# Kernel tuning notes

Measured on AMD Instinct MI355X. Metric: run time of the kernel, lower is better.

## Reference

```python
import jax, jax.numpy as jnp
import numpy as np

NUM_HEADS = 4


def _conv1x1(W, b, x):
    # nn.Conv1d(d_model, d_model, kernel_size=1): pointwise channel mix
    return jnp.einsum('oi,bin->bon', W, x) + b[None, :, None]


def _rot3d_rel_position(desc0, pos, lrf):
    # desc0: [b, d, h, n_pts], pos: [b, n, m, 3], lrf: [b, n, 3, 3] (n == n_pts == m)
    b, d, h, npts = desc0.shape
    m = pos.shape[2]
    # rotate-half: pairs (x0, x1) -> (-x1, x0)
    dh = desc0.reshape(b, d // 2, 2, h, npts)
    desc = jnp.concatenate([-dh[:, :, 1:2], dh[:, :, 0:1]], axis=2).reshape(b, d, h, npts)
    # rotate relative positions into each point's local reference frame
    # torch: einsum('bnxy,bnmy->bnmx', lrf.transpose(2,3), pos) == einsum('bnyx,bnmy->bnmx', lrf, pos)
    posl = jnp.einsum('bnyx,bnmy->bnmx', lrf, pos)
    px, py, pz = posl[..., 0], posl[..., 1], posl[..., 2]
    alpha = jnp.arctan(py / px)
    alpha = jnp.where(px < 0, alpha + np.pi, alpha)
    phi = jnp.arctan(pz / jnp.sqrt(px * px + py * py))
    alpha = jnp.where(jnp.isnan(alpha), 0.0, alpha)
    phi = jnp.where(jnp.isnan(phi), 0.0, phi)
    # F.interpolate(nearest, [m,4]) on [b,n,m,2] duplicates the last axis: [a,a,p,p]
    rot = jnp.stack([alpha, alpha, phi, phi], axis=-1)      # [b,n,m,4]
    rot = jnp.tile(rot, (1, 1, 1, d // 4))                  # [b,n,m,d] (head-independent)
    # 5D rotated value tensor (faithful to original math; head axis broadcast)
    return (jnp.einsum('bdhn,bnmd->bdhnm', desc0, jnp.cos(rot))
            + jnp.einsum('bdhn,bnmd->bdhnm', desc, jnp.sin(rot)))


def setup_inputs() -> dict:
    key = jax.random.key(0)
    ks = jax.random.split(key, 13)
    b, d_model, n, m = 4, 256, 256, 256
    s = 1.0 / np.sqrt(d_model)
    inp = {
        'x': jax.random.normal(ks[0], (b, d_model, n), dtype=jnp.float32),
        'source': jax.random.normal(ks[1], (b, d_model, m), dtype=jnp.float32),
        'x_pos': jax.random.normal(ks[2], (b, n, 3), dtype=jnp.float32),
        'src_pos': jax.random.normal(ks[3], (b, m, 3), dtype=jnp.float32),
        'lrf': jax.random.normal(ks[4], (b, n, 3, 3), dtype=jnp.float32),
        'Wq': jax.random.normal(ks[5], (d_model, d_model), dtype=jnp.float32) * s,
        'bq': jax.random.normal(ks[6], (d_model,), dtype=jnp.float32) * 0.02,
        'Wk': jax.random.normal(ks[7], (d_model, d_model), dtype=jnp.float32) * s,
        'bk': jax.random.normal(ks[8], (d_model,), dtype=jnp.float32) * 0.02,
        'Wv': jax.random.normal(ks[9], (d_model, d_model), dtype=jnp.float32) * s,
        'bv': jax.random.normal(ks[10], (d_model,), dtype=jnp.float32) * 0.02,
        'Wm': jax.random.normal(ks[11], (d_model, d_model), dtype=jnp.float32) * s,
        'bm': jax.random.normal(ks[12], (d_model,), dtype=jnp.float32) * 0.02,
        'k': 32,
    }
    return inp


def reference(x, source, x_pos, src_pos, lrf, Wq, bq, Wk, bk, Wv, bv, Wm, bm, k):
    b, d_model, n = x.shape
    m = source.shape[2]
    h = NUM_HEADS
    dim = d_model // h
    q = _conv1x1(Wq, bq, x).reshape(b, dim, h, n)
    key_ = _conv1x1(Wk, bk, source).reshape(b, dim, h, m)
    val = _conv1x1(Wv, bv, source).reshape(b, dim, h, m)
    # 'self' branch: 3D rotary relative-position encoding of values
    rel = x_pos[:, :, None, :] - src_pos[:, None, :, :]  # [b,n,m,3]
    value5 = _rot3d_rel_position(val, rel, lrf)          # [b,dim,h,n,m]
    # dynamic (top-k sparsified) attention
    scores = jnp.einsum('bdhn,bdhm->bhnm', q, key_) / np.float32(dim) ** 0.5
    vals, idx = jax.lax.top_k(scores, k)                 # over key axis m
    probs = jax.nn.softmax(vals, axis=-1)
    bi = jnp.arange(b)[:, None, None, None]
    hi = jnp.arange(h)[None, :, None, None]
    ni = jnp.arange(n)[None, None, :, None]
    sparse = jnp.zeros_like(scores).at[bi, hi, ni, idx].set(probs)
    # note the deliberate m<->n swap on value5 as in the original einsum
    out = jnp.einsum('bhnm,bdhmn->bdhn', sparse, value5)
    return _conv1x1(Wm, bm, out.reshape(b, d_model, n))
```

## Files before the change

kernel.cpp:

```cpp
#include <hip/hip_runtime.h>
#include <math.h>

#define DM 256
#define NP 256
#define NH 4
#define DH 64

typedef unsigned long long u64;
typedef unsigned int u32;

__global__ __launch_bounds__(256) void qkv_proj_kernel(
    const float* __restrict__ x, const float* __restrict__ src,
    const float* __restrict__ Wq, const float* __restrict__ bq,
    const float* __restrict__ Wk, const float* __restrict__ bk,
    const float* __restrict__ Wv, const float* __restrict__ bv,
    float* __restrict__ Qt, float* __restrict__ Kt, float* __restrict__ Vt)
{
  const int tile = blockIdx.x;
  const int mat  = blockIdx.y;
  const int b    = blockIdx.z;
  const int tc = (tile >> 2) * 64;
  const int tp = (tile & 3) * 64;
  const float* W    = (mat == 0) ? Wq : (mat == 1) ? Wk : Wv;
  const float* bias = (mat == 0) ? bq : (mat == 1) ? bk : bv;
  const float* X    = ((mat == 0) ? x : src) + (size_t)b * DM * NP;
  float* T          = ((mat == 0) ? Qt : (mat == 1) ? Kt : Vt) + (size_t)b * NH * NP * DH;

  __shared__ float Ws[2][32][64];
  __shared__ float Xs[2][32][64];
  const int tid = threadIdx.x;
  const int ty = tid >> 4, tx = tid & 15;
  const int c0 = tid >> 3;
  const int k4 = tid & 7;
  const int pX = tid & 15;
  const int kX = tid >> 4;

  float4 wA, wB, xA, xB;
  #define LOADQKV(K0)                                                          \
    wA = *(const float4*)&W[(size_t)(tc + c0)      * DM + (K0) + k4 * 4];      \
    wB = *(const float4*)&W[(size_t)(tc + c0 + 32) * DM + (K0) + k4 * 4];      \
    xA = *(const float4*)&X[(size_t)((K0) + kX)      * NP + tp + pX * 4];      \
    xB = *(const float4*)&X[(size_t)((K0) + kX + 16) * NP + tp + pX * 4];

  #define STOREQKV(BUF)                                                        \
    Ws[BUF][k4*4+0][c0] = wA.x; Ws[BUF][k4*4+1][c0] = wA.y;                    \
    Ws[BUF][k4*4+2][c0] = wA.z; Ws[BUF][k4*4+3][c0] = wA.w;                    \
    Ws[BUF][k4*4+0][c0+32] = wB.x; Ws[BUF][k4*4+1][c0+32] = wB.y;              \
    Ws[BUF][k4*4+2][c0+32] = wB.z; Ws[BUF][k4*4+3][c0+32] = wB.w;              \
    *(float4*)&Xs[BUF][kX][pX*4]      = xA;                                    \
    *(float4*)&Xs[BUF][kX+16][pX*4]   = xB;

  LOADQKV(0);
  STOREQKV(0);
  __syncthreads();

  float acc[4][4];
  #pragma unroll
  for (int i = 0; i < 4; ++i)
    #pragma unroll
    for (int j = 0; j < 4; ++j) acc[i][j] = 0.f;

  for (int ch = 0; ch < 8; ++ch) {
    const int cur = ch & 1;
    if (ch < 7) { LOADQKV((ch + 1) * 32); }
    #pragma unroll
    for (int kk = 0; kk < 32; ++kk) {
      float4 a = *(const float4*)&Ws[cur][kk][ty * 4];
      float4 xv = *(const float4*)&Xs[cur][kk][tx * 4];
      float av[4] = {a.x, a.y, a.z, a.w};
      float xvv[4] = {xv.x, xv.y, xv.z, xv.w};
      #pragma unroll
      for (int i = 0; i < 4; ++i)
        #pragma unroll
        for (int j = 0; j < 4; ++j) acc[i][j] += av[i] * xvv[j];
    }
    if (ch < 7) {
      STOREQKV(cur ^ 1);
      __syncthreads();
    }
  }

  #pragma unroll
  for (int i = 0; i < 4; ++i) {
    const int c = tc + ty * 4 + i;
    const float bb = bias[c];
    #pragma unroll
    for (int j = 0; j < 4; ++j) {
      const int p = tp + tx * 4 + j;
      T[((size_t)(c & 3) * NP + p) * DH + (c >> 2)] = acc[i][j] + bb;
    }
  }
  #undef LOADQKV
  #undef STOREQKV
}

__global__ __launch_bounds__(256) void score_gemm_kernel(
    const float* __restrict__ Qt, const float* __restrict__ Kt,
    float* __restrict__ scores)
{
  const int tile = blockIdx.x;
  const int bh   = blockIdx.y;
  const int tn = (tile >> 2) * 64;
  const int tm = (tile & 3) * 64;
  const float* Qb = Qt + (size_t)bh * NP * DH;
  const float* Kb = Kt + (size_t)bh * NP * DH;

  __shared__ float Qs[64][68];
  __shared__ float Ks[64][68];
  const int tid = threadIdx.x;

  #pragma unroll
  for (int p = 0; p < 4; ++p) {
    const int u = tid + p * 256;
    const int r = u >> 4;
    const int g = u & 15;
    const float4 qv = *(const float4*)&Qb[(size_t)(tn + r) * DH + g * 4];
    const float4 kv = *(const float4*)&Kb[(size_t)(tm + r) * DH + g * 4];
    Qs[g*4+0][r] = qv.x; Qs[g*4+1][r] = qv.y;
    Qs[g*4+2][r] = qv.z; Qs[g*4+3][r] = qv.w;
    Ks[g*4+0][r] = kv.x; Ks[g*4+1][r] = kv.y;
    Ks[g*4+2][r] = kv.z; Ks[g*4+3][r] = kv.w;
  }
  __syncthreads();

  const int ty = tid >> 4, tx = tid & 15;
  float acc[4][4];
  #pragma unroll
  for (int i = 0; i < 4; ++i)
    #pragma unroll
    for (int j = 0; j < 4; ++j) acc[i][j] = 0.f;

  #pragma unroll 4
  for (int d = 0; d < DH; ++d) {
    const float4 a = *(const float4*)&Qs[d][ty * 4];
    const float4 bv = *(const float4*)&Ks[d][tx * 4];
    const float av[4] = {a.x, a.y, a.z, a.w};
    const float bvv[4] = {bv.x, bv.y, bv.z, bv.w};
    #pragma unroll
    for (int i = 0; i < 4; ++i)
      #pragma unroll
      for (int j = 0; j < 4; ++j) acc[i][j] += av[i] * bvv[j];
  }

  float* srow = scores + ((size_t)bh * NP + tn) * NP + tm;
  #pragma unroll
  for (int i = 0; i < 4; ++i) {
    float4 o4;
    o4.x = acc[i][0] * 0.125f; o4.y = acc[i][1] * 0.125f;
    o4.z = acc[i][2] * 0.125f; o4.w = acc[i][3] * 0.125f;
    *(float4*)&srow[(size_t)(ty * 4 + i) * NP + tx * 4] = o4;
  }
}

__global__ __launch_bounds__(256) void attn_topk_kernel(
    const float* __restrict__ scores, const float* __restrict__ Vt,
    const float* __restrict__ x_pos, const float* __restrict__ src_pos,
    const float* __restrict__ lrf,
    const int* __restrict__ kptr,
    float* __restrict__ O)
{
  const int tid  = threadIdx.x;
  const int wid  = tid >> 6;
  const int lane = tid & 63;
  const int bidx = blockIdx.x;
  const int rb   = (bidx & 7) * 128 + (bidx >> 3);
  const int row  = rb * 4 + wid;
  const int n    = row & (NP - 1);
  const int bh   = row >> 8;
  const int b    = bh >> 2;
  const int h    = bh & 3;

  int kk = *kptr;
  if (kk > 64) kk = 64;
  if (kk < 1) kk = 1;

  __shared__ float  eslot[4][64];
  __shared__ int    msel[4][64];
  __shared__ float4 ang[4][64];
  __shared__ float  otile[4][64];

  const float4 s4 = *(const float4*)&scores[(size_t)row * NP + lane * 4];
  float s[4] = { s4.x, s4.y, s4.z, s4.w };
  u32 u[4], lowv[4];
  #pragma unroll
  for (int r = 0; r < 4; ++r) {
    u32 bb = __float_as_uint(s[r]);
    u[r] = (bb & 0x80000000u) ? ~bb : (bb | 0x80000000u);
    lowv[r] = (u32)(255 - (lane * 4 + r));
  }

  u32 T = 0u;
  #pragma unroll
  for (int bit = 31; bit >= 0; --bit) {
    const u32 cand = T | (1u << bit);
    int c = 0;
    #pragma unroll
    for (int r = 0; r < 4; ++r) c += __popcll(__ballot(u[r] >= cand));
    if (c >= kk) T = cand;
  }
  int c_gt = 0;
  #pragma unroll
  for (int r = 0; r < 4; ++r) c_gt += __popcll(__ballot(u[r] > T));

  u32 Lo = 0u;
  #pragma unroll
  for (int bit = 7; bit >= 0; --bit) {
    const u32 cand = Lo | (1u << bit);
    int c = c_gt;
    #pragma unroll
    for (int r = 0; r < 4; ++r)
      c += __popcll(__ballot((u[r] == T) && (lowv[r] >= cand)));
    if (c >= kk) Lo = cand;
  }

  const float sT = __uint_as_float((T & 0x80000000u) ? (T & 0x7fffffffu) : ~T);
  bool sel[4]; float e[4]; u64 selm[4];
  #pragma unroll
  for (int r = 0; r < 4; ++r) {
    sel[r] = (u[r] > T) || ((u[r] == T) && (lowv[r] >= Lo));
    e[r] = sel[r] ? expf(s[r] - sT) : 0.f;
    selm[r] = __ballot(sel[r]);
  }
  float z = e[0] + e[1] + e[2] + e[3];
  #pragma unroll
  for (int off = 32; off; off >>= 1) z += __shfl_xor(z, off);

  const u64 lt = (1ull << lane) - 1ull;
  int base = 0;
  #pragma unroll
  for (int r = 0; r < 4; ++r) {
    if (sel[r]) {
      const int slot = base + __popcll(selm[r] & lt);
      eslot[wid][slot] = e[r];
      msel[wid][slot]  = lane * 4 + r;
    }
    base += __popcll(selm[r]);
  }

  if (lane < kk) {
    const float ej = eslot[wid][lane];
    const int   mj = msel[wid][lane];
    const float p = ej / z;
    const float* xp = x_pos   + ((size_t)b * NP + mj) * 3;
    const float* sp = src_pos + ((size_t)b * NP + n) * 3;
    const float* L  = lrf     + ((size_t)b * NP + mj) * 9;
    const float r0 = xp[0] - sp[0], r1 = xp[1] - sp[1], r2v = xp[2] - sp[2];
    const float px = L[0]*r0 + L[3]*r1 + L[6]*r2v;
    const float py = L[1]*r0 + L[4]*r1 + L[7]*r2v;
    const float pz = L[2]*r0 + L[5]*r1 + L[8]*r2v;
    const float r2 = px*px + py*py;
    const float inv2 = (r2 > 0.f) ? rsqrtf(r2) : 0.f;
    const float ca = (r2 > 0.f) ? px * inv2 : 1.f;
    const float sa = py * inv2;
    const float r2d = r2 * inv2;
    const float r3 = r2 + pz * pz;
    const float inv3 = (r3 > 0.f) ? rsqrtf(r3) : 0.f;
    const float cph = (r3 > 0.f) ? r2d * inv3 : 1.f;
    const float sph = pz * inv3;
    ang[wid][lane] = make_float4(p * ca, p * sa, p * cph, p * sph);
  }

  const float* vbase = Vt + (size_t)bh * NP * DH;
  const bool useA = ((lane & 3) < 2);
  const bool odd  = (lane & 1);
  const int  ev   = lane & ~1;
  float acc = 0.f;

  int j = 0;
  for (; j + 4 <= kk; j += 4) {
    const int ma = msel[wid][j],   mb = msel[wid][j+1];
    const int mc = msel[wid][j+2], md = msel[wid][j+3];
    const float4 Aa = ang[wid][j],   Ab = ang[wid][j+1];
    const float4 Ac = ang[wid][j+2], Ad = ang[wid][j+3];
    const float2 va = *(const float2*)(vbase + (size_t)ma * DH + ev);
    const float2 vb = *(const float2*)(vbase + (size_t)mb * DH + ev);
    const float2 vc = *(const float2*)(vbase + (size_t)mc * DH + ev);
    const float2 vd = *(const float2*)(vbase + (size_t)md * DH + ev);
    float vm, dsc, pc, ps;
    vm = odd ? va.y : va.x;  dsc = odd ? va.x : -va.y;
    pc = useA ? Aa.x : Aa.z; ps  = useA ? Aa.y : Aa.w;
    acc += vm * pc + dsc * ps;
    vm = odd ? vb.y : vb.x;  dsc = odd ? vb.x : -vb.y;
    pc = useA ? Ab.x : Ab.z; ps  = useA ? Ab.y : Ab.w;
    acc += vm * pc + dsc * ps;
    vm = odd ? vc.y : vc.x;  dsc = odd ? vc.x : -vc.y;
    pc = useA ? Ac.x : Ac.z; ps  = useA ? Ac.y : Ac.w;
    acc += vm * pc + dsc * ps;
    vm = odd ? vd.y : vd.x;  dsc = odd ? vd.x : -vd.y;
    pc = useA ? Ad.x : Ad.z; ps  = useA ? Ad.y : Ad.w;
    acc += vm * pc + dsc * ps;
  }
  for (; j < kk; ++j) {
    const int m = msel[wid][j];
    const float4 A = ang[wid][j];
    const float2 v2 = *(const float2*)(vbase + (size_t)m * DH + ev);
    const float vm  = odd ? v2.y :  v2.x;
    const float dsc = odd ? v2.x : -v2.y;
    acc += vm * (useA ? A.x : A.z) + dsc * (useA ? A.y : A.w);
  }

  otile[wid][lane] = acc;
  __syncthreads();
  if (wid == 0) {
    float4 o4;
    o4.x = otile[0][lane]; o4.y = otile[1][lane];
    o4.z = otile[2][lane]; o4.w = otile[3][lane];
    const int c = (lane << 2) | h;
    const int n0 = (rb * 4) & (NP - 1);
    *(float4*)&O[((size_t)b * DM + c) * NP + n0] = o4;
  }
}

__global__ __launch_bounds__(256) void final_proj_kernel(
    const float* __restrict__ O, const float* __restrict__ Wm,
    const float* __restrict__ bm, float* __restrict__ out)
{
  const int tile = blockIdx.x;
  const int b    = blockIdx.y;
  const int tc = (tile >> 2) * 64;
  const int tp = (tile & 3) * 64;
  const float* X = O + (size_t)b * DM * NP;
  float* Y       = out + (size_t)b * DM * NP;

  __shared__ float Ws[2][32][64];
  __shared__ float Xs[2][32][64];
  const int tid = threadIdx.x;
  const int ty = tid >> 4, tx = tid & 15;
  const int c0 = tid >> 3;
  const int k4 = tid & 7;
  const int pX = tid & 15;
  const int kX = tid >> 4;

  float4 wA, wB, xA, xB;
  #define LOADF(K0)                                                            \
    wA = *(const float4*)&Wm[(size_t)(tc + c0)      * DM + (K0) + k4 * 4];     \
    wB = *(const float4*)&Wm[(size_t)(tc + c0 + 32) * DM + (K0) + k4 * 4];     \
    xA = *(const float4*)&X[(size_t)((K0) + kX)      * NP + tp + pX * 4];      \
    xB = *(const float4*)&X[(size_t)((K0) + kX + 16) * NP + tp + pX * 4];

  #define STOREF(BUF)                                                          \
    Ws[BUF][k4*4+0][c0] = wA.x; Ws[BUF][k4*4+1][c0] = wA.y;                    \
    Ws[BUF][k4*4+2][c0] = wA.z; Ws[BUF][k4*4+3][c0] = wA.w;                    \
    Ws[BUF][k4*4+0][c0+32] = wB.x; Ws[BUF][k4*4+1][c0+32] = wB.y;              \
    Ws[BUF][k4*4+2][c0+32] = wB.z; Ws[BUF][k4*4+3][c0+32] = wB.w;              \
    *(float4*)&Xs[BUF][kX][pX*4]      = xA;                                    \
    *(float4*)&Xs[BUF][kX+16][pX*4]   = xB;

  LOADF(0);
  STOREF(0);
  __syncthreads();

  float acc[4][4];
  #pragma unroll
  for (int i = 0; i < 4; ++i)
    #pragma unroll
    for (int j = 0; j < 4; ++j) acc[i][j] = 0.f;

  for (int ch = 0; ch < 8; ++ch) {
    const int cur = ch & 1;
    if (ch < 7) { LOADF((ch + 1) * 32); }
    #pragma unroll
    for (int kk = 0; kk < 32; ++kk) {
      float4 a = *(const float4*)&Ws[cur][kk][ty * 4];
      float4 xv = *(const float4*)&Xs[cur][kk][tx * 4];
      float av[4] = {a.x, a.y, a.z, a.w};
      float xvv[4] = {xv.x, xv.y, xv.z, xv.w};
      #pragma unroll
      for (int i = 0; i < 4; ++i)
        #pragma unroll
        for (int j = 0; j < 4; ++j) acc[i][j] += av[i] * xvv[j];
    }
    if (ch < 7) {
      STOREF(cur ^ 1);
      __syncthreads();
    }
  }

  #pragma unroll
  for (int i = 0; i < 4; ++i) {
    const int c = tc + ty * 4 + i;
    const float bb = bm[c];
    float4 o4;
    o4.x = acc[i][0] + bb; o4.y = acc[i][1] + bb;
    o4.z = acc[i][2] + bb; o4.w = acc[i][3] + bb;
    *(float4*)&Y[(size_t)c * NP + tp + tx * 4] = o4;
  }
  #undef LOADF
  #undef STOREF
}

extern "C" void kernel_launch(void* const* d_in, const int* in_sizes, int n_in,
                              void* d_out, int out_size, void* d_ws, size_t ws_size,
                              hipStream_t stream)
{
  const float* x       = (const float*)d_in[0];
  const float* source  = (const float*)d_in[1];
  const float* x_pos   = (const float*)d_in[2];
  const float* src_pos = (const float*)d_in[3];
  const float* lrf     = (const float*)d_in[4];
  const float* Wq = (const float*)d_in[5];
  const float* bq = (const float*)d_in[6];
  const float* Wk = (const float*)d_in[7];
  const float* bk = (const float*)d_in[8];
  const float* Wv = (const float*)d_in[9];
  const float* bv = (const float*)d_in[10];
  const float* Wm = (const float*)d_in[11];
  const float* bm = (const float*)d_in[12];
  const int* kptr = (const int*)d_in[13];
  float* out = (float*)d_out;

  float* ws = (float*)d_ws;
  float* Qt = ws;
  float* Kt = Qt + 262144;
  float* Vt = Kt + 262144;
  float* O  = Vt + 262144;
  float* scores = O + 262144;

  qkv_proj_kernel<<<dim3(16, 3, 4), 256, 0, stream>>>(
      x, source, Wq, bq, Wk, bk, Wv, bv, Qt, Kt, Vt);
  score_gemm_kernel<<<dim3(16, 16), 256, 0, stream>>>(
      Qt, Kt, scores);
  attn_topk_kernel<<<dim3(1024), 256, 0, stream>>>(
      scores, Vt, x_pos, src_pos, lrf, kptr, O);
  final_proj_kernel<<<dim3(16, 4), 256, 0, stream>>>(
      O, Wm, bm, out);
}
```

Measured before the change: 52.46 us.

## Fuse four kernels into one persistent kernel with grid-wide barriers

Replaces the four separate launches (QKV projection, score GEMM, top-k attention, output projection) with one 256-block persistent kernel that separates phases with atomic-counter grid barriers, and a union of shared-memory layouts per phase. The aim is to remove inter-kernel launch gaps and tail effects. It also retiles the final projection to 32x32 tiles so it spans all 256 blocks, skips the tie-break bit search when there are no ties, and reuses the Qt buffer for O. The cost is a memset launch plus spin-wait barriers, which assume all 256 blocks are co-resident and can deadlock if they are not.

```diff
diff --git a/kernel.cpp b/kernel.cpp
--- a/kernel.cpp
+++ b/kernel.cpp
@@ -5,388 +5,387 @@
 #define NP 256
 #define NH 4
 #define DH 64
+#define NBLK 256
 
 typedef unsigned long long u64;
 typedef unsigned int u32;
 
-__global__ __launch_bounds__(256) void qkv_proj_kernel(
+union SMem {
+  struct { float Ws[2][32][64]; float Xs[2][32][64]; } p1;
+  struct { float Qs[64][68]; float Ks[64][68]; } p2;
+  struct { float eslot[4][64]; int msel[4][64];
+           float4 ang[4][64]; float otile[4][64]; } p3;
+  struct { float Wc[2][32][32]; float Xc[2][32][32]; } p4;
+};
+
+__device__ __forceinline__ void grid_barrier(int* bar, int idx) {
+  __syncthreads();
+  if (threadIdx.x == 0) {
+    __threadfence();
+    atomicAdd(&bar[idx], 1);
+    while (__hip_atomic_load(&bar[idx], __ATOMIC_ACQUIRE,
+                             __HIP_MEMORY_SCOPE_AGENT) < NBLK) { }
+  }
+  __syncthreads();
+  __threadfence();
+}
+
+__global__ __launch_bounds__(256, 1) void mega_kernel(
     const float* __restrict__ x, const float* __restrict__ src,
     const float* __restrict__ Wq, const float* __restrict__ bq,
     const float* __restrict__ Wk, const float* __restrict__ bk,
     const float* __restrict__ Wv, const float* __restrict__ bv,
-    float* __restrict__ Qt, float* __restrict__ Kt, float* __restrict__ Vt)
+    const float* __restrict__ Wm, const float* __restrict__ bm,
+    const float* __restrict__ x_pos, const float* __restrict__ src_pos,
+    const float* __restrict__ lrf, const int* __restrict__ kptr,
+    float* __restrict__ Qt, float* __restrict__ Kt, float* __restrict__ Vt,
+    float* __restrict__ scores, float* __restrict__ O,
+    int* __restrict__ bar,
+    float* __restrict__ out)
 {
-  const int tile = blockIdx.x;
-  const int mat  = blockIdx.y;
-  const int b    = blockIdx.z;
-  const int tc = (tile >> 2) * 64;
-  const int tp = (tile & 3) * 64;
-  const float* W    = (mat == 0) ? Wq : (mat == 1) ? Wk : Wv;
-  const float* bias = (mat == 0) ? bq : (mat == 1) ? bk : bv;
-  const float* X    = ((mat == 0) ? x : src) + (size_t)b * DM * NP;
-  float* T          = ((mat == 0) ? Qt : (mat == 1) ? Kt : Vt) + (size_t)b * NH * NP * DH;
-
-  __shared__ float Ws[2][32][64];
-  __shared__ float Xs[2][32][64];
+  __shared__ SMem S;
   const int tid = threadIdx.x;
-  const int ty = tid >> 4, tx = tid & 15;
-  const int c0 = tid >> 3;
-  const int k4 = tid & 7;
-  const int pX = tid & 15;
-  const int kX = tid >> 4;
-
-  float4 wA, wB, xA, xB;
-  #define LOADQKV(K0)                                                          \
-    wA = *(const float4*)&W[(size_t)(tc + c0)      * DM + (K0) + k4 * 4];      \
-    wB = *(const float4*)&W[(size_t)(tc + c0 + 32) * DM + (K0) + k4 * 4];      \
-    xA = *(const float4*)&X[(size_t)((K0) + kX)      * NP + tp + pX * 4];      \
-    xB = *(const float4*)&X[(size_t)((K0) + kX + 16) * NP + tp + pX * 4];
-
-  #define STOREQKV(BUF)                                                        \
-    Ws[BUF][k4*4+0][c0] = wA.x; Ws[BUF][k4*4+1][c0] = wA.y;                    \
-    Ws[BUF][k4*4+2][c0] = wA.z; Ws[BUF][k4*4+3][c0] = wA.w;                    \
-    Ws[BUF][k4*4+0][c0+32] = wB.x; Ws[BUF][k4*4+1][c0+32] = wB.y;              \
-    Ws[BUF][k4*4+2][c0+32] = wB.z; Ws[BUF][k4*4+3][c0+32] = wB.w;              \
-    *(float4*)&Xs[BUF][kX][pX*4]      = xA;                                    \
-    *(float4*)&Xs[BUF][kX+16][pX*4]   = xB;
-
-  LOADQKV(0);
-  STOREQKV(0);
-  __syncthreads();
-
-  float acc[4][4];
-  #pragma unroll
-  for (int i = 0; i < 4; ++i)
+  const int bid = blockIdx.x;
+
+  if (bid < 192) {
+    const int tile = bid & 15;
+    const int r    = bid >> 4;
+    const int mat  = r % 3;
+    const int b    = r / 3;
+    const int tc = (tile >> 2) * 64;
+    const int tp = (tile & 3) * 64;
+    const float* W    = (mat == 0) ? Wq : (mat == 1) ? Wk : Wv;
+    const float* bias = (mat == 0) ? bq : (mat == 1) ? bk : bv;
+    const float* X    = ((mat == 0) ? x : src) + (size_t)b * DM * NP;
+    float* T          = ((mat == 0) ? Qt : (mat == 1) ? Kt : Vt)
+                        + (size_t)b * NH * NP * DH;
+
+    const int ty = tid >> 4, tx = tid & 15;
+    const int c0 = tid >> 3;
+    const int k4 = tid & 7;
+    const int pX = tid & 15;
+    const int kX = tid >> 4;
+
+    float4 wA, wB, xA, xB;
+    #define LOADQKV(K0)                                                        \
+      wA = *(const float4*)&W[(size_t)(tc + c0)      * DM + (K0) + k4 * 4];    \
+      wB = *(const float4*)&W[(size_t)(tc + c0 + 32) * DM + (K0) + k4 * 4];    \
+      xA = *(const float4*)&X[(size_t)((K0) + kX)      * NP + tp + pX * 4];    \
+      xB = *(const float4*)&X[(size_t)((K0) + kX + 16) * NP + tp + pX * 4];
+    #define STOREQKV(BUF)                                                      \
+      S.p1.Ws[BUF][k4*4+0][c0] = wA.x; S.p1.Ws[BUF][k4*4+1][c0] = wA.y;        \
+      S.p1.Ws[BUF][k4*4+2][c0] = wA.z; S.p1.Ws[BUF][k4*4+3][c0] = wA.w;        \
+      S.p1.Ws[BUF][k4*4+0][c0+32] = wB.x; S.p1.Ws[BUF][k4*4+1][c0+32] = wB.y;  \
+      S.p1.Ws[BUF][k4*4+2][c0+32] = wB.z; S.p1.Ws[BUF][k4*4+3][c0+32] = wB.w;  \
+      *(float4*)&S.p1.Xs[BUF][kX][pX*4]    = xA;                               \
+      *(float4*)&S.p1.Xs[BUF][kX+16][pX*4] = xB;
+
+    LOADQKV(0);
+    STOREQKV(0);
+    __syncthreads();
+
+    float acc[4][4];
     #pragma unroll
-    for (int j = 0; j < 4; ++j) acc[i][j] = 0.f;
-
-  for (int ch = 0; ch < 8; ++ch) {
-    const int cur = ch & 1;
-    if (ch < 7) { LOADQKV((ch + 1) * 32); }
+    for (int i = 0; i < 4; ++i)
+      #pragma unroll
+      for (int j = 0; j < 4; ++j) acc[i][j] = 0.f;
+
+    for (int ch = 0; ch < 8; ++ch) {
+      const int cur = ch & 1;
+      if (ch < 7) { LOADQKV((ch + 1) * 32); }
+      #pragma unroll
+      for (int kx = 0; kx < 32; ++kx) {
+        float4 a  = *(const float4*)&S.p1.Ws[cur][kx][ty * 4];
+        float4 xv = *(const float4*)&S.p1.Xs[cur][kx][tx * 4];
+        float av[4]  = {a.x, a.y, a.z, a.w};
+        float xvv[4] = {xv.x, xv.y, xv.z, xv.w};
+        #pragma unroll
+        for (int i = 0; i < 4; ++i)
+          #pragma unroll
+          for (int j = 0; j < 4; ++j) acc[i][j] += av[i] * xvv[j];
+      }
+      if (ch < 7) {
+        STOREQKV(cur ^ 1);
+        __syncthreads();
+      }
+    }
+
     #pragma unroll
-    for (int kk = 0; kk < 32; ++kk) {
-      float4 a = *(const float4*)&Ws[cur][kk][ty * 4];
-      float4 xv = *(const float4*)&Xs[cur][kk][tx * 4];
-      float av[4] = {a.x, a.y, a.z, a.w};
-      float xvv[4] = {xv.x, xv.y, xv.z, xv.w};
+    for (int i = 0; i < 4; ++i) {
+      const int c = tc + ty * 4 + i;
+      const float bb = bias[c];
+      #pragma unroll
+      for (int j = 0; j < 4; ++j) {
+        const int p = tp + tx * 4 + j;
+        T[((size_t)(c & 3) * NP + p) * DH + (c >> 2)] = acc[i][j] + bb;
+      }
+    }
+    #undef LOADQKV
+    #undef STOREQKV
+  }
+
+  grid_barrier(bar, 0);
+
+  {
+    const int tile = bid & 15;
+    const int bh   = bid >> 4;
+    const int tn = (tile >> 2) * 64;
+    const int tm = (tile & 3) * 64;
+    const float* Qb = Qt + (size_t)bh * NP * DH;
+    const float* Kb = Kt + (size_t)bh * NP * DH;
+
+    #pragma unroll
+    for (int p = 0; p < 4; ++p) {
+      const int u = tid + p * 256;
+      const int r = u >> 4;
+      const int g = u & 15;
+      const float4 qv = *(const float4*)&Qb[(size_t)(tn + r) * DH + g * 4];
+      const float4 kv = *(const float4*)&Kb[(size_t)(tm + r) * DH + g * 4];
+      S.p2.Qs[g*4+0][r] = qv.x; S.p2.Qs[g*4+1][r] = qv.y;
+      S.p2.Qs[g*4+2][r] = qv.z; S.p2.Qs[g*4+3][r] = qv.w;
+      S.p2.Ks[g*4+0][r] = kv.x; S.p2.Ks[g*4+1][r] = kv.y;
+      S.p2.Ks[g*4+2][r] = kv.z; S.p2.Ks[g*4+3][r] = kv.w;
+    }
+    __syncthreads();
+
+    const int ty = tid >> 4, tx = tid & 15;
+    float acc[4][4];
+    #pragma unroll
+    for (int i = 0; i < 4; ++i)
+      #pragma unroll
+      for (int j = 0; j < 4; ++j) acc[i][j] = 0.f;
+
+    #pragma unroll 4
+    for (int d = 0; d < DH; ++d) {
+      const float4 a  = *(const float4*)&S.p2.Qs[d][ty * 4];
+      const float4 bv = *(const float4*)&S.p2.Ks[d][tx * 4];
+      const float av[4]  = {a.x, a.y, a.z, a.w};
+      const float bvv[4] = {bv.x, bv.y, bv.z, bv.w};
       #pragma unroll
       for (int i = 0; i < 4; ++i)
         #pragma unroll
-        for (int j = 0; j < 4; ++j) acc[i][j] += av[i] * xvv[j];
-    }
-    if (ch < 7) {
-      STOREQKV(cur ^ 1);
+        for (int j = 0; j < 4; ++j) acc[i][j] += av[i] * bvv[j];
+    }
+
+    float* srow = scores + ((size_t)bh * NP + tn) * NP + tm;
+    #pragma unroll
+    for (int i = 0; i < 4; ++i) {
+      float4 o4;
+      o4.x = acc[i][0] * 0.125f; o4.y = acc[i][1] * 0.125f;
+      o4.z = acc[i][2] * 0.125f; o4.w = acc[i][3] * 0.125f;
+      *(float4*)&srow[(size_t)(ty * 4 + i) * NP + tx * 4] = o4;
+    }
+  }
+
+  grid_barrier(bar, 1);
+
+  {
+    const int wid  = tid >> 6;
+    const int lane = tid & 63;
+    int kk = *kptr;
+    if (kk > 64) kk = 64;
+    if (kk < 1) kk = 1;
+
+    for (int sweep = 0; sweep < 4; ++sweep) {
+      const int rb  = sweep * 256 + bid;
+      const int row = rb * 4 + wid;
+      const int n   = row & (NP - 1);
+      const int bh  = row >> 8;
+      const int b   = bh >> 2;
+      const int h   = bh & 3;
+
+      const float4 s4 = *(const float4*)&scores[(size_t)row * NP + lane * 4];
+      float s[4] = { s4.x, s4.y, s4.z, s4.w };
+      u32 u[4], lowv[4];
+      #pragma unroll
+      for (int r = 0; r < 4; ++r) {
+        u32 bb = __float_as_uint(s[r]);
+        u[r] = (bb & 0x80000000u) ? ~bb : (bb | 0x80000000u);
+        lowv[r] = (u32)(255 - (lane * 4 + r));
+      }
+
+      u32 T = 0u;
+      #pragma unroll
+      for (int bit = 31; bit >= 0; --bit) {
+        const u32 cand = T | (1u << bit);
+        int c = 0;
+        #pragma unroll
+        for (int r = 0; r < 4; ++r) c += __popcll(__ballot(u[r] >= cand));
+        if (c >= kk) T = cand;
+      }
+      int c_gt = 0, c_ge = 0;
+      #pragma unroll
+      for (int r = 0; r < 4; ++r) {
+        c_gt += __popcll(__ballot(u[r] > T));
+        c_ge += __popcll(__ballot(u[r] >= T));
+      }
+
+      u32 Lo = 0u;
+      if (c_ge > kk) {
+        #pragma unroll
+        for (int bit = 7; bit >= 0; --bit) {
+          const u32 cand = Lo | (1u << bit);
+          int c = c_gt;
+          #pragma unroll
+          for (int r = 0; r < 4; ++r)
+            c += __popcll(__ballot((u[r] == T) && (lowv[r] >= cand)));
+          if (c >= kk) Lo = cand;
+        }
+      }
+
+      const float sT = __uint_as_float((T & 0x80000000u) ? (T & 0x7fffffffu) : ~T);
+      bool sel[4]; float e[4]; u64 selm[4];
+      #pragma unroll
+      for (int r = 0; r < 4; ++r) {
+        sel[r] = (u[r] > T) || ((u[r] == T) && (lowv[r] >= Lo));
+        e[r] = sel[r] ? expf(s[r] - sT) : 0.f;
+        selm[r] = __ballot(sel[r]);
+      }
+      float z = e[0] + e[1] + e[2] + e[3];
+      #pragma unroll
+      for (int off = 32; off; off >>= 1) z += __shfl_xor(z, off);
+
+      const u64 lt = (1ull << lane) - 1ull;
+      int base = 0;
+      #pragma unroll
+      for (int r = 0; r < 4; ++r) {
+        if (sel[r]) {
+          const int slot = base + __popcll(selm[r] & lt);
+          S.p3.eslot[wid][slot] = e[r];
+          S.p3.msel[wid][slot]  = lane * 4 + r;
+        }
+        base += __popcll(selm[r]);
+      }
+
+      if (lane < kk) {
+        const float ej = S.p3.eslot[wid][lane];
+        const int   mj = S.p3.msel[wid][lane];
+        const float p = ej / z;
+        const float* xp = x_pos   + ((size_t)b * NP + mj) * 3;
+        const float* sp = src_pos + ((size_t)b * NP + n) * 3;
+        const float* L  = lrf     + ((size_t)b * NP + mj) * 9;
+        const float r0 = xp[0] - sp[0], r1 = xp[1] - sp[1], r2v = xp[2] - sp[2];
+        const float px = L[0]*r0 + L[3]*r1 + L[6]*r2v;
+        const float py = L[1]*r0 + L[4]*r1 + L[7]*r2v;
+        const float pz = L[2]*r0 + L[5]*r1 + L[8]*r2v;
+        const float r2 = px*px + py*py;
+        const float inv2 = (r2 > 0.f) ? rsqrtf(r2) : 0.f;
+        const float ca = (r2 > 0.f) ? px * inv2 : 1.f;
+        const float sa = py * inv2;
+        const float r2d = r2 * inv2;
+        const float r3 = r2 + pz * pz;
+        const float inv3 = (r3 > 0.f) ? rsqrtf(r3) : 0.f;
+        const float cph = (r3 > 0.f) ? r2d * inv3 : 1.f;
+        const float sph = pz * inv3;
+        S.p3.ang[wid][lane] = make_float4(p * ca, p * sa, p * cph, p * sph);
+      }
+
+      const float* vbase = Vt + (size_t)bh * NP * DH;
+      const bool useA = ((lane & 3) < 2);
+      const bool odd  = (lane & 1);
+      const int  ev   = lane & ~1;
+      float acc = 0.f;
+
+      int j = 0;
+      for (; j + 4 <= kk; j += 4) {
+        const int ma = S.p3.msel[wid][j],   mb2 = S.p3.msel[wid][j+1];
+        const int mc = S.p3.msel[wid][j+2], md = S.p3.msel[wid][j+3];
+        const float4 Aa = S.p3.ang[wid][j],   Ab = S.p3.ang[wid][j+1];
+        const float4 Ac = S.p3.ang[wid][j+2], Ad = S.p3.ang[wid][j+3];
+        const float2 va = *(const float2*)(vbase + (size_t)ma  * DH + ev);
+        const float2 vb = *(const float2*)(vbase + (size_t)mb2 * DH + ev);
+        const float2 vc = *(const float2*)(vbase + (size_t)mc  * DH + ev);
+        const float2 vd = *(const float2*)(vbase + (size_t)md  * DH + ev);
+        float vm, dsc, pc, ps;
+        vm = odd ? va.y : va.x;  dsc = odd ? va.x : -va.y;
+        pc = useA ? Aa.x : Aa.z; ps  = useA ? Aa.y : Aa.w;
+        acc += vm * pc + dsc * ps;
+        vm = odd ? vb.y : vb.x;  dsc = odd ? vb.x : -vb.y;
+        pc = useA ? Ab.x : Ab.z; ps  = useA ? Ab.y : Ab.w;
+        acc += vm * pc + dsc * ps;
+        vm = odd ? vc.y : vc.x;  dsc = odd ? vc.x : -vc.y;
+        pc = useA ? Ac.x : Ac.z; ps  = useA ? Ac.y : Ac.w;
+        acc += vm * pc + dsc * ps;
+        vm = odd ? vd.y : vd.x;  dsc = odd ? vd.x : -vd.y;
+        pc = useA ? Ad.x : Ad.z; ps  = useA ? Ad.y : Ad.w;
+        acc += vm * pc + dsc * ps;
+      }
+      for (; j < kk; ++j) {
+        const int m = S.p3.msel[wid][j];
+        const float4 A = S.p3.ang[wid][j];
+        const float2 v2 = *(const float2*)(vbase + (size_t)m * DH + ev);
+        const float vm  = odd ? v2.y :  v2.x;
+        const float dsc = odd ? v2.x : -v2.y;
+        acc += vm * (useA ? A.x : A.z) + dsc * (useA ? A.y : A.w);
+      }
+
+      S.p3.otile[wid][lane] = acc;
       __syncthreads();
+      if (wid == 0) {
+        float4 o4;
+        o4.x = S.p3.otile[0][lane]; o4.y = S.p3.otile[1][lane];
+        o4.z = S.p3.otile[2][lane]; o4.w = S.p3.otile[3][lane];
+        const int c = (lane << 2) | h;
+        const int n0 = (rb * 4) & (NP - 1);
+        *(float4*)&O[((size_t)b * DM + c) * NP + n0] = o4;
+      }
+      __syncthreads();
     }
   }
 
-  #pragma unroll
-  for (int i = 0; i < 4; ++i) {
-    const int c = tc + ty * 4 + i;
-    const float bb = bias[c];
-    #pragma unroll
-    for (int j = 0; j < 4; ++j) {
-      const int p = tp + tx * 4 + j;
-      T[((size_t)(c & 3) * NP + p) * DH + (c >> 2)] = acc[i][j] + bb;
-    }
+  grid_barrier(bar, 2);
+
+  {
+    const int tp = (bid & 7) * 32;
+    const int tc = ((bid >> 3) & 7) * 32;
+    const int b  = bid >> 6;
+    const float* X = O + (size_t)b * DM * NP;
+    float* Y       = out + (size_t)b * DM * NP;
+
+    const int c0w = tid >> 3, kg = tid & 7;
+    const int krx = tid >> 3, pg = tid & 7;
+    const int ty = tid >> 4, tx = tid & 15;
+
+    float4 wv4, xv4;
+    #define LOADP4(K0)                                                         \
+      wv4 = *(const float4*)&Wm[(size_t)(tc + c0w) * DM + (K0) + kg * 4];      \
+      xv4 = *(const float4*)&X[(size_t)((K0) + krx) * NP + tp + pg * 4];
+    #define STOREP4(BUF)                                                       \
+      S.p4.Wc[BUF][kg*4+0][c0w] = wv4.x; S.p4.Wc[BUF][kg*4+1][c0w] = wv4.y;    \
+      S.p4.Wc[BUF][kg*4+2][c0w] = wv4.z; S.p4.Wc[BUF][kg*4+3][c0w] = wv4.w;    \
+      *(float4*)&S.p4.Xc[BUF][krx][pg*4] = xv4;
+
+    LOADP4(0);
+    STOREP4(0);
+    __syncthreads();
+
+    float a00 = 0.f, a01 = 0.f, a10 = 0.f, a11 = 0.f;
+    for (int ch = 0; ch < 8; ++ch) {
+      const int cur = ch & 1;
+      if (ch < 7) { LOADP4((ch + 1) * 32); }
+      #pragma unroll
+      for (int kx = 0; kx < 32; ++kx) {
+        const float2 wv = *(const float2*)&S.p4.Wc[cur][kx][ty * 2];
+        const float2 xv = *(const float2*)&S.p4.Xc[cur][kx][tx * 2];
+        a00 += wv.x * xv.x; a01 += wv.x * xv.y;
+        a10 += wv.y * xv.x; a11 += wv.y * xv.y;
+      }
+      if (ch < 7) {
+        STOREP4(cur ^ 1);
+        __syncthreads();
+      }
+    }
+
+    const int c = tc + ty * 2;
+    const int p = tp + tx * 2;
+    const float b0 = bm[c], b1 = bm[c + 1];
+    float2 o0 = make_float2(a00 + b0, a01 + b0);
+    float2 o1 = make_float2(a10 + b1, a11 + b1);
+    *(float2*)&Y[(size_t)c       * NP + p] = o0;
+    *(float2*)&Y[(size_t)(c + 1) * NP + p] = o1;
+    #undef LOADP4
+    #undef STOREP4
   }
-  #undef LOADQKV
-  #undef STOREQKV
-}
-
-__global__ __launch_bounds__(256) void score_gemm_kernel(
-    const float* __restrict__ Qt, const float* __restrict__ Kt,
-    float* __restrict__ scores)
-{
-  const int tile = blockIdx.x;
-  const int bh   = blockIdx.y;
-  const int tn = (tile >> 2) * 64;
-  const int tm = (tile & 3) * 64;
-  const float* Qb = Qt + (size_t)bh * NP * DH;
-  const float* Kb = Kt + (size_t)bh * NP * DH;
-
-  __shared__ float Qs[64][68];
-  __shared__ float Ks[64][68];
-  const int tid = threadIdx.x;
-
-  #pragma unroll
-  for (int p = 0; p < 4; ++p) {
-    const int u = tid + p * 256;
-    const int r = u >> 4;
-    const int g = u & 15;
-    const float4 qv = *(const float4*)&Qb[(size_t)(tn + r) * DH + g * 4];
-    const float4 kv = *(const float4*)&Kb[(size_t)(tm + r) * DH + g * 4];
-    Qs[g*4+0][r] = qv.x; Qs[g*4+1][r] = qv.y;
-    Qs[g*4+2][r] = qv.z; Qs[g*4+3][r] = qv.w;
-    Ks[g*4+0][r] = kv.x; Ks[g*4+1][r] = kv.y;
-    Ks[g*4+2][r] = kv.z; Ks[g*4+3][r] = kv.w;
-  }
-  __syncthreads();
-
-  const int ty = tid >> 4, tx = tid & 15;
-  float acc[4][4];
-  #pragma unroll
-  for (int i = 0; i < 4; ++i)
-    #pragma unroll
-    for (int j = 0; j < 4; ++j) acc[i][j] = 0.f;
-
-  #pragma unroll 4
-  for (int d = 0; d < DH; ++d) {
-    const float4 a = *(const float4*)&Qs[d][ty * 4];
-    const float4 bv = *(const float4*)&Ks[d][tx * 4];
-    const float av[4] = {a.x, a.y, a.z, a.w};
-    const float bvv[4] = {bv.x, bv.y, bv.z, bv.w};
-    #pragma unroll
-    for (int i = 0; i < 4; ++i)
-      #pragma unroll
-      for (int j = 0; j < 4; ++j) acc[i][j] += av[i] * bvv[j];
-  }
-
-  float* srow = scores + ((size_t)bh * NP + tn) * NP + tm;
-  #pragma unroll
-  for (int i = 0; i < 4; ++i) {
-    float4 o4;
-    o4.x = acc[i][0] * 0.125f; o4.y = acc[i][1] * 0.125f;
-    o4.z = acc[i][2] * 0.125f; o4.w = acc[i][3] * 0.125f;
-    *(float4*)&srow[(size_t)(ty * 4 + i) * NP + tx * 4] = o4;
-  }
-}
-
-__global__ __launch_bounds__(256) void attn_topk_kernel(
-    const float* __restrict__ scores, const float* __restrict__ Vt,
-    const float* __restrict__ x_pos, const float* __restrict__ src_pos,
-    const float* __restrict__ lrf,
-    const int* __restrict__ kptr,
-    float* __restrict__ O)
-{
-  const int tid  = threadIdx.x;
-  const int wid  = tid >> 6;
-  const int lane = tid & 63;
-  const int bidx = blockIdx.x;
-  const int rb   = (bidx & 7) * 128 + (bidx >> 3);
-  const int row  = rb * 4 + wid;
-  const int n    = row & (NP - 1);
-  const int bh   = row >> 8;
-  const int b    = bh >> 2;
-  const int h    = bh & 3;
-
-  int kk = *kptr;
-  if (kk > 64) kk = 64;
-  if (kk < 1) kk = 1;
-
-  __shared__ float  eslot[4][64];
-  __shared__ int    msel[4][64];
-  __shared__ float4 ang[4][64];
-  __shared__ float  otile[4][64];
-
-  const float4 s4 = *(const float4*)&scores[(size_t)row * NP + lane * 4];
-  float s[4] = { s4.x, s4.y, s4.z, s4.w };
-  u32 u[4], lowv[4];
-  #pragma unroll
-  for (int r = 0; r < 4; ++r) {
-    u32 bb = __float_as_uint(s[r]);
-    u[r] = (bb & 0x80000000u) ? ~bb : (bb | 0x80000000u);
-    lowv[r] = (u32)(255 - (lane * 4 + r));
-  }
-
-  u32 T = 0u;
-  #pragma unroll
-  for (int bit = 31; bit >= 0; --bit) {
-    const u32 cand = T | (1u << bit);
-    int c = 0;
-    #pragma unroll
-    for (int r = 0; r < 4; ++r) c += __popcll(__ballot(u[r] >= cand));
-    if (c >= kk) T = cand;
-  }
-  int c_gt = 0;
-  #pragma unroll
-  for (int r = 0; r < 4; ++r) c_gt += __popcll(__ballot(u[r] > T));
-
-  u32 Lo = 0u;
-  #pragma unroll
-  for (int bit = 7; bit >= 0; --bit) {
-    const u32 cand = Lo | (1u << bit);
-    int c = c_gt;
-    #pragma unroll
-    for (int r = 0; r < 4; ++r)
-      c += __popcll(__ballot((u[r] == T) && (lowv[r] >= cand)));
-    if (c >= kk) Lo = cand;
-  }
-
-  const float sT = __uint_as_float((T & 0x80000000u) ? (T & 0x7fffffffu) : ~T);
-  bool sel[4]; float e[4]; u64 selm[4];
-  #pragma unroll
-  for (int r = 0; r < 4; ++r) {
-    sel[r] = (u[r] > T) || ((u[r] == T) && (lowv[r] >= Lo));
-    e[r] = sel[r] ? expf(s[r] - sT) : 0.f;
-    selm[r] = __ballot(sel[r]);
-  }
-  float z = e[0] + e[1] + e[2] + e[3];
-  #pragma unroll
-  for (int off = 32; off; off >>= 1) z += __shfl_xor(z, off);
-
-  const u64 lt = (1ull << lane) - 1ull;
-  int base = 0;
-  #pragma unroll
-  for (int r = 0; r < 4; ++r) {
-    if (sel[r]) {
-      const int slot = base + __popcll(selm[r] & lt);
-      eslot[wid][slot] = e[r];
-      msel[wid][slot]  = lane * 4 + r;
-    }
-    base += __popcll(selm[r]);
-  }
-
-  if (lane < kk) {
-    const float ej = eslot[wid][lane];
-    const int   mj = msel[wid][lane];
-    const float p = ej / z;
-    const float* xp = x_pos   + ((size_t)b * NP + mj) * 3;
-    const float* sp = src_pos + ((size_t)b * NP + n) * 3;
-    const float* L  = lrf     + ((size_t)b * NP + mj) * 9;
-    const float r0 = xp[0] - sp[0], r1 = xp[1] - sp[1], r2v = xp[2] - sp[2];
-    const float px = L[0]*r0 + L[3]*r1 + L[6]*r2v;
-    const float py = L[1]*r0 + L[4]*r1 + L[7]*r2v;
-    const float pz = L[2]*r0 + L[5]*r1 + L[8]*r2v;
-    const float r2 = px*px + py*py;
-    const float inv2 = (r2 > 0.f) ? rsqrtf(r2) : 0.f;
-    const float ca = (r2 > 0.f) ? px * inv2 : 1.f;
-    const float sa = py * inv2;
-    const float r2d = r2 * inv2;
-    const float r3 = r2 + pz * pz;
-    const float inv3 = (r3 > 0.f) ? rsqrtf(r3) : 0.f;
-    const float cph = (r3 > 0.f) ? r2d * inv3 : 1.f;
-    const float sph = pz * inv3;
-    ang[wid][lane] = make_float4(p * ca, p * sa, p * cph, p * sph);
-  }
-
-  const float* vbase = Vt + (size_t)bh * NP * DH;
-  const bool useA = ((lane & 3) < 2);
-  const bool odd  = (lane & 1);
-  const int  ev   = lane & ~1;
-  float acc = 0.f;
-
-  int j = 0;
-  for (; j + 4 <= kk; j += 4) {
-    const int ma = msel[wid][j],   mb = msel[wid][j+1];
-    const int mc = msel[wid][j+2], md = msel[wid][j+3];
-    const float4 Aa = ang[wid][j],   Ab = ang[wid][j+1];
-    const float4 Ac = ang[wid][j+2], Ad = ang[wid][j+3];
-    const float2 va = *(const float2*)(vbase + (size_t)ma * DH + ev);
-    const float2 vb = *(const float2*)(vbase + (size_t)mb * DH + ev);
-    const float2 vc = *(const float2*)(vbase + (size_t)mc * DH + ev);
-    const float2 vd = *(const float2*)(vbase + (size_t)md * DH + ev);
-    float vm, dsc, pc, ps;
-    vm = odd ? va.y : va.x;  dsc = odd ? va.x : -va.y;
-    pc = useA ? Aa.x : Aa.z; ps  = useA ? Aa.y : Aa.w;
-    acc += vm * pc + dsc * ps;
-    vm = odd ? vb.y : vb.x;  dsc = odd ? vb.x : -vb.y;
-    pc = useA ? Ab.x : Ab.z; ps  = useA ? Ab.y : Ab.w;
-    acc += vm * pc + dsc * ps;
-    vm = odd ? vc.y : vc.x;  dsc = odd ? vc.x : -vc.y;
-    pc = useA ? Ac.x : Ac.z; ps  = useA ? Ac.y : Ac.w;
-    acc += vm * pc + dsc * ps;
-    vm = odd ? vd.y : vd.x;  dsc = odd ? vd.x : -vd.y;
-    pc = useA ? Ad.x : Ad.z; ps  = useA ? Ad.y : Ad.w;
-    acc += vm * pc + dsc * ps;
-  }
-  for (; j < kk; ++j) {
-    const int m = msel[wid][j];
-    const float4 A = ang[wid][j];
-    const float2 v2 = *(const float2*)(vbase + (size_t)m * DH + ev);
-    const float vm  = odd ? v2.y :  v2.x;
-    const float dsc = odd ? v2.x : -v2.y;
-    acc += vm * (useA ? A.x : A.z) + dsc * (useA ? A.y : A.w);
-  }
-
-  otile[wid][lane] = acc;
-  __syncthreads();
-  if (wid == 0) {
-    float4 o4;
-    o4.x = otile[0][lane]; o4.y = otile[1][lane];
-    o4.z = otile[2][lane]; o4.w = otile[3][lane];
-    const int c = (lane << 2) | h;
-    const int n0 = (rb * 4) & (NP - 1);
-    *(float4*)&O[((size_t)b * DM + c) * NP + n0] = o4;
-  }
-}
-
-__global__ __launch_bounds__(256) void final_proj_kernel(
-    const float* __restrict__ O, const float* __restrict__ Wm,
-    const float* __restrict__ bm, float* __restrict__ out)
-{
-  const int tile = blockIdx.x;
-  const int b    = blockIdx.y;
-  const int tc = (tile >> 2) * 64;
-  const int tp = (tile & 3) * 64;
-  const float* X = O + (size_t)b * DM * NP;
-  float* Y       = out + (size_t)b * DM * NP;
-
-  __shared__ float Ws[2][32][64];
-  __shared__ float Xs[2][32][64];
-  const int tid = threadIdx.x;
-  const int ty = tid >> 4, tx = tid & 15;
-  const int c0 = tid >> 3;
-  const int k4 = tid & 7;
-  const int pX = tid & 15;
-  const int kX = tid >> 4;
-
-  float4 wA, wB, xA, xB;
-  #define LOADF(K0)                                                            \
-    wA = *(const float4*)&Wm[(size_t)(tc + c0)      * DM + (K0) + k4 * 4];     \
-    wB = *(const float4*)&Wm[(size_t)(tc + c0 + 32) * DM + (K0) + k4 * 4];     \
-    xA = *(const float4*)&X[(size_t)((K0) + kX)      * NP + tp + pX * 4];      \
-    xB = *(const float4*)&X[(size_t)((K0) + kX + 16) * NP + tp + pX * 4];
-
-  #define STOREF(BUF)                                                          \
-    Ws[BUF][k4*4+0][c0] = wA.x; Ws[BUF][k4*4+1][c0] = wA.y;                    \
-    Ws[BUF][k4*4+2][c0] = wA.z; Ws[BUF][k4*4+3][c0] = wA.w;                    \
-    Ws[BUF][k4*4+0][c0+32] = wB.x; Ws[BUF][k4*4+1][c0+32] = wB.y;              \
-    Ws[BUF][k4*4+2][c0+32] = wB.z; Ws[BUF][k4*4+3][c0+32] = wB.w;              \
-    *(float4*)&Xs[BUF][kX][pX*4]      = xA;                                    \
-    *(float4*)&Xs[BUF][kX+16][pX*4]   = xB;
-
-  LOADF(0);
-  STOREF(0);
-  __syncthreads();
-
-  float acc[4][4];
-  #pragma unroll
-  for (int i = 0; i < 4; ++i)
-    #pragma unroll
-    for (int j = 0; j < 4; ++j) acc[i][j] = 0.f;
-
-  for (int ch = 0; ch < 8; ++ch) {
-    const int cur = ch & 1;
-    if (ch < 7) { LOADF((ch + 1) * 32); }
-    #pragma unroll
-    for (int kk = 0; kk < 32; ++kk) {
-      float4 a = *(const float4*)&Ws[cur][kk][ty * 4];
-      float4 xv = *(const float4*)&Xs[cur][kk][tx * 4];
-      float av[4] = {a.x, a.y, a.z, a.w};
-      float xvv[4] = {xv.x, xv.y, xv.z, xv.w};
-      #pragma unroll
-      for (int i = 0; i < 4; ++i)
-        #pragma unroll
-        for (int j = 0; j < 4; ++j) acc[i][j] += av[i] * xvv[j];
-    }
-    if (ch < 7) {
-      STOREF(cur ^ 1);
-      __syncthreads();
-    }
-  }
-
-  #pragma unroll
-  for (int i = 0; i < 4; ++i) {
-    const int c = tc + ty * 4 + i;
-    const float bb = bm[c];
-    float4 o4;
-    o4.x = acc[i][0] + bb; o4.y = acc[i][1] + bb;
-    o4.z = acc[i][2] + bb; o4.w = acc[i][3] + bb;
-    *(float4*)&Y[(size_t)c * NP + tp + tx * 4] = o4;
-  }
-  #undef LOADF
-  #undef STOREF
 }
 
 extern "C" void kernel_launch(void* const* d_in, const int* in_sizes, int n_in,
@@ -413,15 +412,13 @@
   float* Qt = ws;
   float* Kt = Qt + 262144;
   float* Vt = Kt + 262144;
-  float* O  = Vt + 262144;
-  float* scores = O + 262144;
-
-  qkv_proj_kernel<<<dim3(16, 3, 4), 256, 0, stream>>>(
-      x, source, Wq, bq, Wk, bk, Wv, bv, Qt, Kt, Vt);
-  score_gemm_kernel<<<dim3(16, 16), 256, 0, stream>>>(
-      Qt, Kt, scores);
-  attn_topk_kernel<<<dim3(1024), 256, 0, stream>>>(
-      scores, Vt, x_pos, src_pos, lrf, kptr, O);
-  final_proj_kernel<<<dim3(16, 4), 256, 0, stream>>>(
-      O, Wm, bm, out);
+  float* scores = Vt + 262144;
+  int*   bar = (int*)(scores + 1048576);
+  float* O  = Qt;
+
+  hipMemsetAsync(bar, 0, 64, stream);
+  mega_kernel<<<dim3(NBLK), 256, 0, stream>>>(
+      x, source, Wq, bq, Wk, bk, Wv, bv, Wm, bm,
+      x_pos, src_pos, lrf, kptr,
+      Qt, Kt, Vt, scores, O, bar, out);
 }
```

Measured after the change: 182.4 us. 248% more time.
